# Performance work log

Measured on AMD Instinct MI355X. Metric: run time of the kernel, lower is better.

Reference implementation:

```python
import jax, jax.numpy as jnp
import numpy as np

K_TOP = 32
ALPHA = 1.0


def setup_inputs() -> dict:
    key = jax.random.key(0)
    k1, k2, k3 = jax.random.split(key, 3)
    x = jax.random.normal(k1, (1, 512, 1024), dtype=jnp.float32)
    keys = jax.random.normal(k2, (200000, 1024), dtype=jnp.float32) * 0.02
    vals = jax.random.normal(k3, (200000, 1024), dtype=jnp.float32)
    return {"x": x, "keys": keys, "vals": vals}


def reference(x, keys, vals):
    B, L, D = x.shape
    q = x.reshape(B * L, D)                       # [N, D]
    scores = q @ keys.T                           # [N, num_slots] dense matmul
    topv, topi = jax.lax.top_k(scores, K_TOP)     # [N, k]
    attn = jax.nn.softmax(topv, axis=-1)          # [N, k]
    sel_vals = vals[topi]                         # [N, k, D] gather
    out = jnp.einsum('nk,nkd->nd', attn, sel_vals)
    return ALPHA * out.reshape(B, L, D)
```

## Files before the change

kernel.cpp:

```cpp
#include <hip/hip_runtime.h>
#include <hip/hip_bf16.h>
#include <stdint.h>


#define KTOP 32
#define MROWS 512
#define NKEYS 200000
#define DDIM 1024

#define BN2 64
#define BK 64
#define LDT 72
#define NSTEP 16
#define NCOLT2 3125
#define NT2 3136
#define TCAP 512
#define CCAP 256
#define TMARGIN 0.125f

typedef __attribute__((ext_vector_type(4))) float f32x4;
typedef __attribute__((ext_vector_type(8))) short short8;

__device__ __forceinline__ unsigned short f2bf(float f) {
    __hip_bfloat16 h = __float2bfloat16(f);
    return *reinterpret_cast<unsigned short*>(&h);
}
__device__ __forceinline__ int enc16(unsigned short u) {
    return (int)(u ^ ((u & 0x8000u) ? 0xFFFFu : 0x8000u));
}
__device__ __forceinline__ float dec_enc(int e) {
    unsigned short u = (unsigned short)((e & 0x8000) ? (e ^ 0x8000) : (e ^ 0xFFFF));
    return __uint_as_float((unsigned int)u << 16);
}
__device__ __forceinline__ float bf2f(unsigned short u) {
    return __uint_as_float((unsigned int)u << 16);
}

__global__ void cvt_x_kernel(const float* __restrict__ x, unsigned short* __restrict__ xb) {
    int i = blockIdx.x * blockDim.x + threadIdx.x;
    f32x4 v = reinterpret_cast<const f32x4*>(x)[i];
    ushort4 o;
    o.x = f2bf(v.x); o.y = f2bf(v.y); o.z = f2bf(v.z); o.w = f2bf(v.w);
    reinterpret_cast<ushort4*>(xb)[i] = o;
}

__global__ __launch_bounds__(1024, 4)
void score_gemm(const float* __restrict__ keys, const unsigned short* __restrict__ xb,
                unsigned short* __restrict__ scores, unsigned short* __restrict__ tilemax) {
    __shared__ unsigned short As[MROWS * LDT];
    __shared__ unsigned short Bs[BN2 * LDT];
    __shared__ int tmax[MROWS];

    const int tid  = threadIdx.x;
    const int lane = tid & 63;
    const int w    = tid >> 6;

    const int g    = blockIdx.x;
    const int col0 = g * BN2;

    if (tid < MROWS) tmax[tid] = 0;

    f32x4 acc[2][4];
#pragma unroll
    for (int m = 0; m < 2; m++)
#pragma unroll
        for (int n = 0; n < 4; n++) acc[m][n] = (f32x4){0.f, 0.f, 0.f, 0.f};

    short8 areg[4];
    f32x4  breg;

    auto loadA = [&](int k0) {
#pragma unroll
        for (int i = 0; i < 4; i++) {
            int c = i * 1024 + tid;
            int r = c >> 3, j = c & 7;
            areg[i] = *reinterpret_cast<const short8*>(xb + (size_t)r * DDIM + k0 + j * 8);
        }
    };
    auto loadB = [&](int k0) {
        int r = tid >> 4, j = tid & 15;
        breg = *reinterpret_cast<const f32x4*>(keys + (size_t)(col0 + r) * DDIM + k0 + j * 4);
    };
    auto writeLDS = [&]() {
#pragma unroll
        for (int i = 0; i < 4; i++) {
            int c = i * 1024 + tid;
            int r = c >> 3, j = c & 7;
            *reinterpret_cast<short8*>(&As[r * LDT + j * 8]) = areg[i];
        }
        {
            int r = tid >> 4, j = tid & 15;
            ushort4 o;
            o.x = f2bf(breg.x); o.y = f2bf(breg.y);
            o.z = f2bf(breg.z); o.w = f2bf(breg.w);
            *reinterpret_cast<ushort4*>(&Bs[r * LDT + j * 4]) = o;
        }
    };

    const int rl = lane & 15;
    const int kl = (lane >> 4) * 8;

    auto compute = [&]() {
        const unsigned short* Ab = &As[(w * 32 + rl) * LDT + kl];
        const unsigned short* Bb = &Bs[rl * LDT + kl];
#pragma unroll
        for (int kk = 0; kk < BK; kk += 32) {
            short8 af[2], bf[4];
#pragma unroll
            for (int m = 0; m < 2; m++) af[m] = *reinterpret_cast<const short8*>(Ab + m * 16 * LDT + kk);
#pragma unroll
            for (int n = 0; n < 4; n++) bf[n] = *reinterpret_cast<const short8*>(Bb + n * 16 * LDT + kk);
#pragma unroll
            for (int m = 0; m < 2; m++)
#pragma unroll
                for (int n = 0; n < 4; n++)
                    acc[m][n] = __builtin_amdgcn_mfma_f32_16x16x32_bf16(af[m], bf[n], acc[m][n], 0, 0, 0);
        }
    };

    loadA(0); loadB(0);
    for (int t = 0; t < NSTEP; t++) {
        __syncthreads();
        writeLDS();
        __syncthreads();
        if (t + 1 < NSTEP) { loadA((t + 1) * BK); loadB((t + 1) * BK); }
        compute();
    }

    const int rg = lane >> 4;
#pragma unroll
    for (int m = 0; m < 2; m++) {
#pragma unroll
        for (int j = 0; j < 4; j++) {
            int lrow = w * 32 + m * 16 + rg * 4 + j;
            float mx = -1e30f;
#pragma unroll
            for (int n = 0; n < 4; n++) {
                float v = acc[m][n][j];
                mx = fmaxf(mx, v);
                scores[(size_t)lrow * NKEYS + col0 + n * 16 + rl] = f2bf(v);
            }
#pragma unroll
            for (int sft = 1; sft < 16; sft <<= 1) mx = fmaxf(mx, __shfl_xor(mx, sft));
            if (rl == 0)
                atomicMax(&tmax[lrow], enc16(f2bf(mx)));
        }
    }
    __syncthreads();
    if (tid < MROWS)
        tilemax[(size_t)tid * NT2 + g] = (unsigned short)tmax[tid];
}

__global__ __launch_bounds__(256)
void select_kernel(const float* __restrict__ x, const float* __restrict__ keys,
                   const float* __restrict__ vals, const unsigned short* __restrict__ scores,
                   const unsigned short* __restrict__ tilemax, float* __restrict__ out) {
    const int n    = blockIdx.x;
    const int tid  = threadIdx.x;
    const int lane = tid & 63;
    const int w    = tid >> 6;

    __shared__ __align__(16) float qs[DDIM];
    __shared__ unsigned short enc_t[NT2];
    __shared__ int    hist[256];
    __shared__ int    tiles[TCAP];
    __shared__ int    cand[CCAP];
    __shared__ double rsc[CCAP];
    __shared__ float  wgt[KTOP];
    __shared__ int    topslot[KTOP];
    __shared__ float  topval[KTOP];
    __shared__ int    ntiles, ncand, sbsel, sabove, st32e;

    reinterpret_cast<f32x4*>(qs)[tid] = reinterpret_cast<const f32x4*>(x + (size_t)n * DDIM)[tid];
    hist[tid] = 0;
    if (tid < 32) { wgt[tid] = 0.f; topslot[tid] = -1; }
    if (tid == 0) { ntiles = 0; ncand = 0; }
    for (int i = tid; i < NT2; i += 256)
        enc_t[i] = (i < NCOLT2) ? tilemax[(size_t)n * NT2 + i] : 0;
    __syncthreads();

    for (int i = tid; i < NT2; i += 256) atomicAdd(&hist[enc_t[i] >> 8], 1);
    __syncthreads();
    if (tid == 0) {
        int cum = 0, b = 255;
        for (; b >= 0; b--) { cum += hist[b]; if (cum >= KTOP) break; }
        sbsel = b; sabove = cum - hist[b];
    }
    __syncthreads();
    const int bsel = sbsel;
    hist[tid] = 0;
    __syncthreads();
    for (int i = tid; i < NT2; i += 256) {
        int e = enc_t[i];
        if ((e >> 8) == bsel) atomicAdd(&hist[e & 0xFF], 1);
    }
    __syncthreads();
    if (tid == 0) {
        int cum = sabove, lb = 255;
        for (; lb >= 0; lb--) { cum += hist[lb]; if (cum >= KTOP) break; }
        st32e = (bsel << 8) | lb;
    }
    __syncthreads();
    const float thr = dec_enc(st32e) - TMARGIN;

    for (int i = tid; i < NT2; i += 256) {
        if (dec_enc(enc_t[i]) >= thr) {
            int p = atomicAdd(&ntiles, 1);
            if (p < TCAP) tiles[p] = i;
        }
    }
    __syncthreads();
    const int nt = ntiles < TCAP ? ntiles : TCAP;

    for (int idx = tid; idx < nt * BN2; idx += 256) {
        int col = tiles[idx >> 6] * BN2 + (idx & 63);
        float v = bf2f(scores[(size_t)n * NKEYS + col]);
        if (v >= thr) {
            int p = atomicAdd(&ncand, 1);
            if (p < CCAP) cand[p] = col;
        }
    }
    __syncthreads();
    const int cnt = ncand < CCAP ? ncand : CCAP;

    for (int ci = w; ci < cnt; ci += 4) {
        const f32x4* kv = reinterpret_cast<const f32x4*>(keys + (size_t)cand[ci] * DDIM) + lane * 4;
        const f32x4* qv = reinterpret_cast<const f32x4*>(qs) + lane * 4;
        double a = 0.0;
#pragma unroll
        for (int i = 0; i < 4; i++) {
            f32x4 q = qv[i], k = kv[i];
            a += (double)q.x * k.x + (double)q.y * k.y + (double)q.z * k.z + (double)q.w * k.w;
        }
#pragma unroll
        for (int sft = 32; sft >= 1; sft >>= 1) a += __shfl_xor(a, sft);
        if (lane == 0) rsc[ci] = a;
    }
    __syncthreads();

    if (w == 0) {
        double v0[4]; int id0[4];
#pragma unroll
        for (int sft = 0; sft < 4; sft++) {
            int p = lane + sft * 64;
            if (p < cnt) { v0[sft] = rsc[p]; id0[sft] = p; } else { v0[sft] = -1e300; id0[sft] = -1; }
        }
        for (int k = 0; k < KTOP; k++) {
            double bv = v0[0]; int bi = id0[0];
#pragma unroll
            for (int sft = 1; sft < 4; sft++) if (v0[sft] > bv) { bv = v0[sft]; bi = id0[sft]; }
#pragma unroll
            for (int sft = 32; sft >= 1; sft >>= 1) {
                double ov = __shfl_xor(bv, sft);
                int    oi = __shfl_xor(bi, sft);
                if (ov > bv) { bv = ov; bi = oi; }
            }
            if (lane == 0) { topslot[k] = bi; topval[k] = (float)bv; }
#pragma unroll
            for (int sft = 0; sft < 4; sft++) if (bi >= 0 && id0[sft] == bi) v0[sft] = -1e300;
        }
    }
    __syncthreads();

    if (tid == 0) {
        float mx = topval[0];
        float sum = 0.f;
        for (int k = 0; k < KTOP; k++) {
            float e = (topslot[k] >= 0) ? expf(topval[k] - mx) : 0.f;
            wgt[k] = e; sum += e;
        }
        float inv = 1.f / sum;
        for (int k = 0; k < KTOP; k++) wgt[k] *= inv;
    }
    __syncthreads();

    f32x4 accv = (f32x4){0.f, 0.f, 0.f, 0.f};
    for (int k = 0; k < KTOP; k++) {
        int sl = topslot[k];
        if (sl >= 0) {
            float wk = wgt[k];
            f32x4 v = reinterpret_cast<const f32x4*>(vals + (size_t)cand[sl] * DDIM)[tid];
            accv.x += wk * v.x; accv.y += wk * v.y; accv.z += wk * v.z; accv.w += wk * v.w;
        }
    }
    reinterpret_cast<f32x4*>(out + (size_t)n * DDIM)[tid] = accv;
}

extern "C" void kernel_launch(void* const* d_in, const int* in_sizes, int n_in,
                              void* d_out, int out_size, void* d_ws, size_t ws_size,
                              hipStream_t stream) {
    const float* x    = (const float*)d_in[0];
    const float* keys = (const float*)d_in[1];
    const float* vals = (const float*)d_in[2];
    float* out = (float*)d_out;

    char* ws = (char*)d_ws;
    unsigned short* scores  = (unsigned short*)ws;
    unsigned short* xb      = (unsigned short*)(ws + 204800000);
    unsigned short* tilemax = (unsigned short*)(ws + 204800000 + 1048576);

    cvt_x_kernel<<<512, 256, 0, stream>>>(x, xb);
    score_gemm<<<NCOLT2, 1024, 0, stream>>>(keys, xb, scores, tilemax);
    select_kernel<<<MROWS, 256, 0, stream>>>(x, keys, vals, scores, tilemax, out);
}
```

Before: 563.5 us.

## Load query fragments directly from global into registers, drop A shared tile

```diff
diff --git a/kernel.cpp b/kernel.cpp
--- a/kernel.cpp
+++ b/kernel.cpp
@@ -47,7 +47,6 @@
 __global__ __launch_bounds__(1024, 4)
 void score_gemm(const float* __restrict__ keys, const unsigned short* __restrict__ xb,
                 unsigned short* __restrict__ scores, unsigned short* __restrict__ tilemax) {
-    __shared__ unsigned short As[MROWS * LDT];
     __shared__ unsigned short Bs[BN2 * LDT];
     __shared__ int tmax[MROWS];
 
@@ -66,65 +65,63 @@
 #pragma unroll
         for (int n = 0; n < 4; n++) acc[m][n] = (f32x4){0.f, 0.f, 0.f, 0.f};
 
-    short8 areg[4];
-    f32x4  breg;
-
-    auto loadA = [&](int k0) {
-#pragma unroll
-        for (int i = 0; i < 4; i++) {
-            int c = i * 1024 + tid;
-            int r = c >> 3, j = c & 7;
-            areg[i] = *reinterpret_cast<const short8*>(xb + (size_t)r * DDIM + k0 + j * 8);
-        }
-    };
-    auto loadB = [&](int k0) {
-        int r = tid >> 4, j = tid & 15;
-        breg = *reinterpret_cast<const f32x4*>(keys + (size_t)(col0 + r) * DDIM + k0 + j * 4);
-    };
-    auto writeLDS = [&]() {
-#pragma unroll
-        for (int i = 0; i < 4; i++) {
-            int c = i * 1024 + tid;
-            int r = c >> 3, j = c & 7;
-            *reinterpret_cast<short8*>(&As[r * LDT + j * 8]) = areg[i];
-        }
-        {
-            int r = tid >> 4, j = tid & 15;
-            ushort4 o;
-            o.x = f2bf(breg.x); o.y = f2bf(breg.y);
-            o.z = f2bf(breg.z); o.w = f2bf(breg.w);
-            *reinterpret_cast<ushort4*>(&Bs[r * LDT + j * 4]) = o;
-        }
-    };
-
     const int rl = lane & 15;
     const int kl = (lane >> 4) * 8;
 
-    auto compute = [&]() {
-        const unsigned short* Ab = &As[(w * 32 + rl) * LDT + kl];
-        const unsigned short* Bb = &Bs[rl * LDT + kl];
-#pragma unroll
-        for (int kk = 0; kk < BK; kk += 32) {
-            short8 af[2], bf[4];
-#pragma unroll
-            for (int m = 0; m < 2; m++) af[m] = *reinterpret_cast<const short8*>(Ab + m * 16 * LDT + kk);
-#pragma unroll
-            for (int n = 0; n < 4; n++) bf[n] = *reinterpret_cast<const short8*>(Bb + n * 16 * LDT + kk);
+    const unsigned short* Arow0 = xb + (size_t)(w * 32 + rl) * DDIM + kl;
+    const unsigned short* Arow1 = Arow0 + 16 * DDIM;
+
+    short8 af0[2][2], af1[2][2];
+    f32x4  breg0, breg1;
+
+    auto loadA = [&](short8 (&af)[2][2], int t) {
+        const int k0 = t * BK;
+        af[0][0] = *reinterpret_cast<const short8*>(Arow0 + k0);
+        af[0][1] = *reinterpret_cast<const short8*>(Arow0 + k0 + 32);
+        af[1][0] = *reinterpret_cast<const short8*>(Arow1 + k0);
+        af[1][1] = *reinterpret_cast<const short8*>(Arow1 + k0 + 32);
+    };
+    const int br = tid >> 4, bj = tid & 15;
+    auto loadB = [&](f32x4& br_, int t) {
+        br_ = *reinterpret_cast<const f32x4*>(keys + (size_t)(col0 + br) * DDIM + t * BK + bj * 4);
+    };
+    auto writeB = [&](const f32x4& v) {
+        ushort4 o;
+        o.x = f2bf(v.x); o.y = f2bf(v.y);
+        o.z = f2bf(v.z); o.w = f2bf(v.w);
+        *reinterpret_cast<ushort4*>(&Bs[br * LDT + bj * 4]) = o;
+    };
+    auto compute = [&](short8 (&af)[2][2]) {
+#pragma unroll
+        for (int kki = 0; kki < 2; kki++) {
+            short8 bf[4];
+#pragma unroll
+            for (int n = 0; n < 4; n++)
+                bf[n] = *reinterpret_cast<const short8*>(&Bs[(n * 16 + rl) * LDT + kl + kki * 32]);
 #pragma unroll
             for (int m = 0; m < 2; m++)
 #pragma unroll
                 for (int n = 0; n < 4; n++)
-                    acc[m][n] = __builtin_amdgcn_mfma_f32_16x16x32_bf16(af[m], bf[n], acc[m][n], 0, 0, 0);
+                    acc[m][n] = __builtin_amdgcn_mfma_f32_16x16x32_bf16(af[m][kki], bf[n], acc[m][n], 0, 0, 0);
         }
     };
 
-    loadA(0); loadB(0);
-    for (int t = 0; t < NSTEP; t++) {
+    loadB(breg0, 0); loadB(breg1, 1);
+    loadA(af0, 0);
+
+    for (int t = 0; t < NSTEP; t += 2) {
         __syncthreads();
-        writeLDS();
+        writeB(breg0);
         __syncthreads();
-        if (t + 1 < NSTEP) { loadA((t + 1) * BK); loadB((t + 1) * BK); }
-        compute();
+        if (t + 2 < NSTEP) loadB(breg0, t + 2);
+        loadA(af1, t + 1);
+        compute(af0);
+        __syncthreads();
+        writeB(breg1);
+        __syncthreads();
+        if (t + 3 < NSTEP) loadB(breg1, t + 3);
+        if (t + 2 < NSTEP) loadA(af0, t + 2);
+        compute(af1);
     }
 
     const int rg = lane >> 4;
```

Measured after the change: 600.8 us. +6.6%, slower.
